# Optimization experiments

Measured on AMD Instinct MI355X. Metric: run time of the kernel, lower is better.

The kernel has to match this reference:

```python
import jax, jax.numpy as jnp
import numpy as np

N_NODES = 50000
N_EDGES = 800000
D_IN = 128
N_HEAD = 4
D_OUT = D_IN // N_HEAD  # 32


def setup_inputs() -> dict:
    key = jax.random.key(0)
    k1, k2, k3, k4, k5 = jax.random.split(key, 5)
    in_feat = jax.random.normal(k1, (N_NODES, D_IN), dtype=jnp.float32)
    edge_ind = jax.random.randint(k2, (2, N_EDGES), 0, N_NODES, dtype=jnp.int64)
    # xavier-ish scaled params
    W_proj = jax.random.normal(k3, (D_IN, N_HEAD * D_OUT), dtype=jnp.float32) * (1.0 / np.sqrt(D_IN))
    a_src = jax.random.normal(k4, (1, N_HEAD, D_OUT), dtype=jnp.float32) * (1.0 / np.sqrt(D_OUT))
    a_tgt = jax.random.normal(k5, (1, N_HEAD, D_OUT), dtype=jnp.float32) * (1.0 / np.sqrt(D_OUT))
    bias = jnp.zeros((N_HEAD * D_OUT,), dtype=jnp.float32)
    return {"in_feat": in_feat, "edge_ind": edge_ind, "edge_len": N_EDGES,
            "W_proj": W_proj, "a_src": a_src, "a_tgt": a_tgt, "bias": bias}


def reference(in_feat, edge_ind, edge_len, W_proj, a_src, a_tgt, bias):
    n_nodes = in_feat.shape[0]
    n_head, d_out = a_src.shape[1], a_src.shape[2]
    # input projection: [N, d_in] @ [d_in, H*D] -> [N, H, D]
    proj_feat = (in_feat @ W_proj).reshape(n_nodes, n_head, d_out)
    # per-node scores [N, H]
    src_score = jnp.sum(proj_feat * a_src, axis=-1)
    tgt_score = jnp.sum(proj_feat * a_tgt, axis=-1)
    src_ind, tgt_ind = edge_ind[0], edge_ind[1]
    # per-edge score [E, H]
    edge_score = jax.nn.leaky_relu(src_score[src_ind] + tgt_score[tgt_ind], negative_slope=0.2)
    edge_score = jnp.exp(edge_score - jnp.max(edge_score))  # global max, as in source
    # segment-softmax denominator via scatter-add over target nodes
    neigh_sums = jax.ops.segment_sum(edge_score, tgt_ind, num_segments=n_nodes)  # [N, H]
    att_per_edge = edge_score / (neigh_sums[tgt_ind] + 1e-16)  # [E, H]
    # weighted aggregation: gather src features, scale, scatter-add to targets
    src_feat_weighted = proj_feat[src_ind] * att_per_edge[..., None]  # [E, H, D]
    out_feat = jax.ops.segment_sum(src_feat_weighted, tgt_ind, num_segments=n_nodes)  # [N, H, D]
    return out_feat.reshape(n_nodes, -1) + bias
```

## Files before the change

### kernel.cpp

```cpp
#include <hip/hip_runtime.h>
#include <hip/hip_bf16.h>

typedef __attribute__((ext_vector_type(8))) short bf16x8;
typedef __attribute__((ext_vector_type(4))) float f32x4;

__device__ __forceinline__ ushort f2bf(float f) {
    unsigned u = __float_as_uint(f);
    return (ushort)((u + 0x7fffu + ((u >> 16) & 1u)) >> 16);
}
__device__ __forceinline__ float blo(unsigned u) { return __uint_as_float(u << 16); }
__device__ __forceinline__ float bhi(unsigned u) { return __uint_as_float(u & 0xffff0000u); }

__global__ void k_wt(const float* __restrict__ W, ushort* __restrict__ Wt) {
    int idx = blockIdx.x * 256 + threadIdx.x;
    int nn = idx >> 7, kk = idx & 127;
    Wt[idx] = f2bf(W[kk * 128 + nn]);
}

__global__ __launch_bounds__(256) void k_proj(const float* __restrict__ A,
                                              const ushort* __restrict__ Wt_g,
                                              const float* __restrict__ a_src,
                                              const float* __restrict__ a_tgt,
                                              ushort* __restrict__ Pb,
                                              float* __restrict__ ss,
                                              float* __restrict__ ts,
                                              int* __restrict__ deg, int n) {
    __shared__ __align__(16) char smem[49152];
    const int tid = threadIdx.x;
    const int row0 = blockIdx.x * 64;

    {
        int gid = blockIdx.x * 256 + tid;
        if (gid < n) deg[gid] = 0;
    }

#pragma unroll
    for (int it = 0; it < 8; ++it) {
        int idx = it * 256 + tid;
        int r   = idx >> 5;
        int kc  = (idx & 31) << 2;
        int gr  = row0 + r;
        float4 v = make_float4(0.f, 0.f, 0.f, 0.f);
        if (gr < n) v = *(const float4*)&A[(size_t)gr * 128 + kc];
        ushort4 pk;
        pk.x = f2bf(v.x); pk.y = f2bf(v.y); pk.z = f2bf(v.z); pk.w = f2bf(v.w);
        *(ushort4*)(smem + ((r * 256 + kc * 2) ^ ((r & 7) << 4))) = pk;
    }
#pragma unroll
    for (int it = 0; it < 8; ++it) {
        int idx = it * 256 + tid;
        int nn  = idx >> 4;
        int k8  = (idx & 15) << 3;
        uint4 v = *(const uint4*)&Wt_g[nn * 128 + k8];
        *(uint4*)(smem + 16384 + ((nn * 256 + k8 * 2) ^ ((nn & 7) << 4))) = v;
    }
    __syncthreads();

    const int l  = tid & 63, w = tid >> 6;
    const int lr = l & 15,  lk = l >> 4;
    const int arow = w * 16 + lr;

    f32x4 acc[8] = {};
#pragma unroll
    for (int ks = 0; ks < 4; ++ks) {
        int kk = ks * 32 + lk * 8;
        bf16x8 af = *(const bf16x8*)(smem + ((arow * 256 + kk * 2) ^ ((arow & 7) << 4)));
#pragma unroll
        for (int nt = 0; nt < 8; ++nt) {
            int nn = nt * 16 + lr;
            bf16x8 bf = *(const bf16x8*)(smem + 16384 + ((nn * 256 + kk * 2) ^ ((nn & 7) << 4)));
            acc[nt] = __builtin_amdgcn_mfma_f32_16x16x32_bf16(af, bf, acc[nt], 0, 0, 0);
        }
    }

#pragma unroll
    for (int nt = 0; nt < 8; ++nt) {
#pragma unroll
        for (int r = 0; r < 4; ++r) {
            int gr = row0 + w * 16 + lk * 4 + r;
            if (gr < n) Pb[(size_t)gr * 128 + nt * 16 + lr] = f2bf(acc[nt][r]);
        }
    }

    float av[8], bw[8];
#pragma unroll
    for (int t = 0; t < 8; ++t) { av[t] = a_src[t * 16 + lr]; bw[t] = a_tgt[t * 16 + lr]; }
#pragma unroll
    for (int r = 0; r < 4; ++r) {
#pragma unroll
        for (int h = 0; h < 4; ++h) {
            float s1 = acc[2 * h][r] * av[2 * h] + acc[2 * h + 1][r] * av[2 * h + 1];
            float s2 = acc[2 * h][r] * bw[2 * h] + acc[2 * h + 1][r] * bw[2 * h + 1];
#pragma unroll
            for (int off = 1; off < 16; off <<= 1) {
                s1 += __shfl_xor(s1, off, 64);
                s2 += __shfl_xor(s2, off, 64);
            }
            if (lr == 0) {
                int gr = row0 + w * 16 + lk * 4 + r;
                if (gr < n) { ss[gr * 4 + h] = s1; ts[gr * 4 + h] = s2; }
            }
        }
    }
}

__global__ void k_hist(const int* __restrict__ tgt, int* __restrict__ deg,
                       int* __restrict__ rank, int E) {
    int e = blockIdx.x * 256 + threadIdx.x;
    if (e < E) rank[e] = atomicAdd(&deg[tgt[e]], 1);
}

__global__ __launch_bounds__(256) void k_scan1(const int* __restrict__ deg,
                                               int* __restrict__ rowptr,
                                               int* __restrict__ sums, int n) {
    __shared__ int sd[256];
    int tid = threadIdx.x;
    int i = blockIdx.x * 256 + tid;
    int v = (i < n) ? deg[i] : 0;
    sd[tid] = v; __syncthreads();
#pragma unroll
    for (int off = 1; off < 256; off <<= 1) {
        int t = (tid >= off) ? sd[tid - off] : 0;
        __syncthreads();
        sd[tid] += t;
        __syncthreads();
    }
    if (i < n) rowptr[i + 1] = sd[tid];
    if (tid == 255) sums[blockIdx.x] = sd[255];
}

__global__ __launch_bounds__(256) void k_scan23(int* __restrict__ rowptr,
                                                const int* __restrict__ sums,
                                                int nchunks, int n) {
    __shared__ int sd[256];
    int tid = threadIdx.x;
    int v = (tid < nchunks) ? sums[tid] : 0;
    sd[tid] = v; __syncthreads();
#pragma unroll
    for (int off = 1; off < 256; off <<= 1) {
        int t = (tid >= off) ? sd[tid - off] : 0;
        __syncthreads();
        sd[tid] += t;
        __syncthreads();
    }
    int b = blockIdx.x;
    int prefix = (b == 0) ? 0 : sd[b - 1];
    int i = b * 256 + tid;
    if (i < n) {
        rowptr[i + 1] += prefix;
        if (i == 0) rowptr[0] = 0;
    }
}

__global__ void k_scatter(const int* __restrict__ src, const int* __restrict__ tgt,
                          const int* __restrict__ rowptr, const int* __restrict__ rank,
                          int* __restrict__ srcs, int E) {
    int e = blockIdx.x * 256 + threadIdx.x;
    if (e >= E) return;
    int t = tgt[e];
    srcs[rowptr[t] + rank[e]] = src[e];
}

__global__ __launch_bounds__(256) void k_aggr(const int* __restrict__ rowptr,
                                              const int* __restrict__ srcs,
                                              const float* __restrict__ ss,
                                              const float* __restrict__ ts,
                                              const ushort* __restrict__ Pb,
                                              const float* __restrict__ bias,
                                              float* __restrict__ out, int n) {
    int node = blockIdx.x * 4 + (threadIdx.x >> 6);
    if (node >= n) return;
    const int lane = threadIdx.x & 63;
    const int c = lane * 2;
    const int h = lane >> 4;
    const float tsc = ts[node * 4 + h];
    int b0 = rowptr[node], b1 = rowptr[node + 1];

    float ax0 = 0.f, ay0 = 0.f, ax1 = 0.f, ay1 = 0.f;
    float ax2 = 0.f, ay2 = 0.f, ax3 = 0.f, ay3 = 0.f;
    float den = 0.f;
    int i = b0;
    for (; i + 3 < b1; i += 4) {
        int s0 = srcs[i], s1 = srcs[i + 1], s2 = srcs[i + 2], s3 = srcs[i + 3];
        float w0 = ss[s0 * 4 + h] + tsc;
        float w1 = ss[s1 * 4 + h] + tsc;
        float w2 = ss[s2 * 4 + h] + tsc;
        float w3 = ss[s3 * 4 + h] + tsc;
        unsigned p0 = *(const unsigned*)&Pb[(size_t)s0 * 128 + c];
        unsigned p1 = *(const unsigned*)&Pb[(size_t)s1 * 128 + c];
        unsigned p2 = *(const unsigned*)&Pb[(size_t)s2 * 128 + c];
        unsigned p3 = *(const unsigned*)&Pb[(size_t)s3 * 128 + c];
        w0 = w0 > 0.f ? w0 : 0.2f * w0;  float e0 = __expf(w0);
        w1 = w1 > 0.f ? w1 : 0.2f * w1;  float e1 = __expf(w1);
        w2 = w2 > 0.f ? w2 : 0.2f * w2;  float e2 = __expf(w2);
        w3 = w3 > 0.f ? w3 : 0.2f * w3;  float e3 = __expf(w3);
        den += (e0 + e1) + (e2 + e3);
        ax0 = fmaf(e0, blo(p0), ax0); ay0 = fmaf(e0, bhi(p0), ay0);
        ax1 = fmaf(e1, blo(p1), ax1); ay1 = fmaf(e1, bhi(p1), ay1);
        ax2 = fmaf(e2, blo(p2), ax2); ay2 = fmaf(e2, bhi(p2), ay2);
        ax3 = fmaf(e3, blo(p3), ax3); ay3 = fmaf(e3, bhi(p3), ay3);
    }
    for (; i < b1; ++i) {
        int s0 = srcs[i];
        float w0 = ss[s0 * 4 + h] + tsc;
        w0 = w0 > 0.f ? w0 : 0.2f * w0;
        float e0 = __expf(w0);
        unsigned p0 = *(const unsigned*)&Pb[(size_t)s0 * 128 + c];
        den += e0;
        ax0 = fmaf(e0, blo(p0), ax0); ay0 = fmaf(e0, bhi(p0), ay0);
    }
    float inv = 1.f / (den + 1e-16f);
    float2 bv = *(const float2*)&bias[c];
    float2 o;
    o.x = ((ax0 + ax1) + (ax2 + ax3)) * inv + bv.x;
    o.y = ((ay0 + ay1) + (ay2 + ay3)) * inv + bv.y;
    *(float2*)&out[(size_t)node * 128 + c] = o;
}

extern "C" void kernel_launch(void* const* d_in, const int* in_sizes, int n_in,
                              void* d_out, int out_size, void* d_ws, size_t ws_size,
                              hipStream_t stream) {
    const float* in_feat = (const float*)d_in[0];
    const int*   edge    = (const int*)d_in[1];
    const float* W_proj  = (const float*)d_in[3];
    const float* a_src   = (const float*)d_in[4];
    const float* a_tgt   = (const float*)d_in[5];
    const float* bias    = (const float*)d_in[6];
    float* out = (float*)d_out;

    const int n = in_sizes[0] / 128;
    const int E = in_sizes[1] / 2;
    const int* src = edge;
    const int* tgt = edge + E;

    ushort* Pb   = (ushort*)d_ws;
    ushort* Wt_g = Pb + (size_t)n * 128;
    float*  ss   = (float*)(Wt_g + 128 * 128);
    float*  ts   = ss + (size_t)n * 4;
    int* deg    = (int*)(ts + (size_t)n * 4);
    int* rowptr = deg + n;
    int* sums   = rowptr + n + 1;
    int* rank   = sums + 256;
    int* srcs   = rank + E;

    const int nchunks = (n + 255) / 256;

    k_wt<<<64, 256, 0, stream>>>(W_proj, Wt_g);
    k_proj<<<(n + 63) / 64, 256, 0, stream>>>(in_feat, Wt_g, a_src, a_tgt,
                                              Pb, ss, ts, deg, n);
    k_hist<<<(E + 255) / 256, 256, 0, stream>>>(tgt, deg, rank, E);
    k_scan1<<<nchunks, 256, 0, stream>>>(deg, rowptr, sums, n);
    k_scan23<<<nchunks, 256, 0, stream>>>(rowptr, sums, nchunks, n);
    k_scatter<<<(E + 255) / 256, 256, 0, stream>>>(src, tgt, rowptr, rank, srcs, E);
    k_aggr<<<(n + 3) / 4, 256, 0, stream>>>(rowptr, srcs, ss, ts, Pb, bias, out, n);
}
```

Before: 127.1 us.

## Fuse histogram into projection, precompute bf16 edge weights, narrow indices to 16-bit

Zeroing of the degree array moves into the weight-transpose kernel, and the histogram becomes extra blocks of the projection launch, removing one kernel. The rank, sorted-source and per-edge exp-score arrays are stored as 16-bit values. The scatter kernel is sharded by destination position and also writes bf16 edge exp scores in CSR order. Aggregation now splits heads across blocks and edge slots across lanes, reading the precomputed scores instead of recomputing them. This cuts gather traffic and exp work in the hot aggregation loop. In exchange, node count and per-node degree must fit in 16 bits, edge weights lose precision, and the scatter reads its inputs eight times.

Result: slower. 201.6 us (+58.6%).

```diff
diff --git a/kernel.cpp b/kernel.cpp
--- a/kernel.cpp
+++ b/kernel.cpp
@@ -8,31 +8,43 @@
     unsigned u = __float_as_uint(f);
     return (ushort)((u + 0x7fffu + ((u >> 16) & 1u)) >> 16);
 }
+__device__ __forceinline__ float bf2f(ushort b) {
+    return __uint_as_float(((unsigned)b) << 16);
+}
 __device__ __forceinline__ float blo(unsigned u) { return __uint_as_float(u << 16); }
 __device__ __forceinline__ float bhi(unsigned u) { return __uint_as_float(u & 0xffff0000u); }
 
-__global__ void k_wt(const float* __restrict__ W, ushort* __restrict__ Wt) {
+__global__ void k_wt(const float* __restrict__ W, ushort* __restrict__ Wt,
+                     int* __restrict__ deg, int n) {
     int idx = blockIdx.x * 256 + threadIdx.x;
-    int nn = idx >> 7, kk = idx & 127;
-    Wt[idx] = f2bf(W[kk * 128 + nn]);
-}
-
-__global__ __launch_bounds__(256) void k_proj(const float* __restrict__ A,
-                                              const ushort* __restrict__ Wt_g,
-                                              const float* __restrict__ a_src,
-                                              const float* __restrict__ a_tgt,
-                                              ushort* __restrict__ Pb,
-                                              float* __restrict__ ss,
-                                              float* __restrict__ ts,
-                                              int* __restrict__ deg, int n) {
+    if (idx < 16384) {
+        int nn = idx >> 7, kk = idx & 127;
+        Wt[idx] = f2bf(W[kk * 128 + nn]);
+    }
+    if (idx < n) deg[idx] = 0;
+}
+
+__global__ __launch_bounds__(256) void k_projhist(const float* __restrict__ A,
+                                                  const ushort* __restrict__ Wt_g,
+                                                  const float* __restrict__ a_src,
+                                                  const float* __restrict__ a_tgt,
+                                                  ushort* __restrict__ Pb,
+                                                  float* __restrict__ ss,
+                                                  float* __restrict__ ts,
+                                                  const int* __restrict__ tgt,
+                                                  int* __restrict__ deg,
+                                                  ushort* __restrict__ rank,
+                                                  int n, int E, int PB) {
     __shared__ __align__(16) char smem[49152];
     const int tid = threadIdx.x;
+
+    if ((int)blockIdx.x >= PB) {
+        int e = ((int)blockIdx.x - PB) * 256 + tid;
+        if (e < E) rank[e] = (ushort)atomicAdd(&deg[tgt[e]], 1);
+        return;
+    }
+
     const int row0 = blockIdx.x * 64;
-
-    {
-        int gid = blockIdx.x * 256 + tid;
-        if (gid < n) deg[gid] = 0;
-    }
 
 #pragma unroll
     for (int it = 0; it < 8; ++it) {
@@ -104,12 +116,6 @@
     }
 }
 
-__global__ void k_hist(const int* __restrict__ tgt, int* __restrict__ deg,
-                       int* __restrict__ rank, int E) {
-    int e = blockIdx.x * 256 + threadIdx.x;
-    if (e < E) rank[e] = atomicAdd(&deg[tgt[e]], 1);
-}
-
 __global__ __launch_bounds__(256) void k_scan1(const int* __restrict__ deg,
                                                int* __restrict__ rowptr,
                                                int* __restrict__ sums, int n) {
@@ -152,69 +158,87 @@
     }
 }
 
-__global__ void k_scatter(const int* __restrict__ src, const int* __restrict__ tgt,
-                          const int* __restrict__ rowptr, const int* __restrict__ rank,
-                          int* __restrict__ srcs, int E) {
-    int e = blockIdx.x * 256 + threadIdx.x;
-    if (e >= E) return;
-    int t = tgt[e];
-    srcs[rowptr[t] + rank[e]] = src[e];
+__global__ __launch_bounds__(256) void k_scatter(const int* __restrict__ src,
+                                                 const int* __restrict__ tgt,
+                                                 const int* __restrict__ rowptr,
+                                                 const ushort* __restrict__ rank,
+                                                 const float* __restrict__ ss,
+                                                 const float* __restrict__ ts,
+                                                 ushort* __restrict__ srcs,
+                                                 ushort* __restrict__ esc, int E) {
+    const int shard = blockIdx.x & 7;
+    const int base  = (blockIdx.x >> 3) * 2048;
+    const int tid = threadIdx.x;
+#pragma unroll
+    for (int j = 0; j < 8; ++j) {
+        int e = base + j * 256 + tid;
+        if (e < E) {
+            int t = tgt[e];
+            int pos = rowptr[t] + rank[e];
+            bool m_src = (((pos >> 5) & 7) == shard);
+            bool m_esc = (((pos >> 3) & 7) == shard);
+            if (m_src | m_esc) {
+                int s = src[e];
+                if (m_src) srcs[pos] = (ushort)s;
+                if (m_esc) {
+                    float4 a = *(const float4*)&ss[s * 4];
+                    float4 b = *(const float4*)&ts[t * 4];
+                    float v; ushort4 r;
+                    v = a.x + b.x; v = v > 0.f ? v : 0.2f * v; r.x = f2bf(__expf(v));
+                    v = a.y + b.y; v = v > 0.f ? v : 0.2f * v; r.y = f2bf(__expf(v));
+                    v = a.z + b.z; v = v > 0.f ? v : 0.2f * v; r.z = f2bf(__expf(v));
+                    v = a.w + b.w; v = v > 0.f ? v : 0.2f * v; r.w = f2bf(__expf(v));
+                    *(ushort4*)&esc[(size_t)pos * 4] = r;
+                }
+            }
+        }
+    }
 }
 
 __global__ __launch_bounds__(256) void k_aggr(const int* __restrict__ rowptr,
-                                              const int* __restrict__ srcs,
-                                              const float* __restrict__ ss,
-                                              const float* __restrict__ ts,
+                                              const int* __restrict__ deg,
+                                              const ushort* __restrict__ srcs,
+                                              const ushort* __restrict__ esc,
                                               const ushort* __restrict__ Pb,
                                               const float* __restrict__ bias,
                                               float* __restrict__ out, int n) {
-    int node = blockIdx.x * 4 + (threadIdx.x >> 6);
+    const int bid = blockIdx.x;
+    const int h = bid & 3;
+    int node = __builtin_amdgcn_readfirstlane(((bid >> 2) << 2) + (threadIdx.x >> 6));
     if (node >= n) return;
     const int lane = threadIdx.x & 63;
-    const int c = lane * 2;
-    const int h = lane >> 4;
-    const float tsc = ts[node * 4 + h];
-    int b0 = rowptr[node], b1 = rowptr[node + 1];
-
-    float ax0 = 0.f, ay0 = 0.f, ax1 = 0.f, ay1 = 0.f;
-    float ax2 = 0.f, ay2 = 0.f, ax3 = 0.f, ay3 = 0.f;
-    float den = 0.f;
-    int i = b0;
-    for (; i + 3 < b1; i += 4) {
-        int s0 = srcs[i], s1 = srcs[i + 1], s2 = srcs[i + 2], s3 = srcs[i + 3];
-        float w0 = ss[s0 * 4 + h] + tsc;
-        float w1 = ss[s1 * 4 + h] + tsc;
-        float w2 = ss[s2 * 4 + h] + tsc;
-        float w3 = ss[s3 * 4 + h] + tsc;
-        unsigned p0 = *(const unsigned*)&Pb[(size_t)s0 * 128 + c];
-        unsigned p1 = *(const unsigned*)&Pb[(size_t)s1 * 128 + c];
-        unsigned p2 = *(const unsigned*)&Pb[(size_t)s2 * 128 + c];
-        unsigned p3 = *(const unsigned*)&Pb[(size_t)s3 * 128 + c];
-        w0 = w0 > 0.f ? w0 : 0.2f * w0;  float e0 = __expf(w0);
-        w1 = w1 > 0.f ? w1 : 0.2f * w1;  float e1 = __expf(w1);
-        w2 = w2 > 0.f ? w2 : 0.2f * w2;  float e2 = __expf(w2);
-        w3 = w3 > 0.f ? w3 : 0.2f * w3;  float e3 = __expf(w3);
-        den += (e0 + e1) + (e2 + e3);
-        ax0 = fmaf(e0, blo(p0), ax0); ay0 = fmaf(e0, bhi(p0), ay0);
-        ax1 = fmaf(e1, blo(p1), ax1); ay1 = fmaf(e1, bhi(p1), ay1);
-        ax2 = fmaf(e2, blo(p2), ax2); ay2 = fmaf(e2, bhi(p2), ay2);
-        ax3 = fmaf(e3, blo(p3), ax3); ay3 = fmaf(e3, bhi(p3), ay3);
-    }
-    for (; i < b1; ++i) {
-        int s0 = srcs[i];
-        float w0 = ss[s0 * 4 + h] + tsc;
-        w0 = w0 > 0.f ? w0 : 0.2f * w0;
-        float e0 = __expf(w0);
-        unsigned p0 = *(const unsigned*)&Pb[(size_t)s0 * 128 + c];
-        den += e0;
-        ax0 = fmaf(e0, blo(p0), ax0); ay0 = fmaf(e0, bhi(p0), ay0);
-    }
-    float inv = 1.f / (den + 1e-16f);
-    float2 bv = *(const float2*)&bias[c];
-    float2 o;
-    o.x = ((ax0 + ax1) + (ax2 + ax3)) * inv + bv.x;
-    o.y = ((ay0 + ay1) + (ay2 + ay3)) * inv + bv.y;
-    *(float2*)&out[(size_t)node * 128 + c] = o;
+    const int slot = lane >> 4;
+    const int q    = lane & 15;
+    const int cidx = h * 32 + q * 2;
+    const int b0 = rowptr[node];
+    const int limit = b0 + deg[node];
+
+    float ax = 0.f, ay = 0.f, den = 0.f;
+    for (int i = b0; i < limit; i += 8) {
+        int ia = i + slot, ib = i + slot + 4;
+        ushort sa = srcs[ia], sb = srcs[ib];
+        bool va = ia < limit, vb = ib < limit;
+        int ma = va ? (int)sa : 0, mb = vb ? (int)sb : 0;
+        unsigned pa = *(const unsigned*)(Pb + (size_t)ma * 128 + cidx);
+        unsigned pb = *(const unsigned*)(Pb + (size_t)mb * 128 + cidx);
+        ushort ua = esc[ia * 4 + h], ub = esc[ib * 4 + h];
+        float ea = va ? bf2f(ua) : 0.f;
+        float eb = vb ? bf2f(ub) : 0.f;
+        den += ea + eb;
+        ax = fmaf(ea, blo(pa), ax); ay = fmaf(ea, bhi(pa), ay);
+        ax = fmaf(eb, blo(pb), ax); ay = fmaf(eb, bhi(pb), ay);
+    }
+    den += __shfl_xor(den, 16, 64); den += __shfl_xor(den, 32, 64);
+    ax  += __shfl_xor(ax, 16, 64);  ax  += __shfl_xor(ax, 32, 64);
+    ay  += __shfl_xor(ay, 16, 64);  ay  += __shfl_xor(ay, 32, 64);
+    if (slot == 0) {
+        float inv = 1.f / (den + 1e-16f);
+        float2 bv = *(const float2*)&bias[cidx];
+        float2 o;
+        o.x = ax * inv + bv.x;
+        o.y = ay * inv + bv.y;
+        *(float2*)&out[(size_t)node * 128 + cidx] = o;
+    }
 }
 
 extern "C" void kernel_launch(void* const* d_in, const int* in_sizes, int n_in,
@@ -233,24 +257,33 @@
     const int* src = edge;
     const int* tgt = edge + E;
 
-    ushort* Pb   = (ushort*)d_ws;
-    ushort* Wt_g = Pb + (size_t)n * 128;
-    float*  ss   = (float*)(Wt_g + 128 * 128);
-    float*  ts   = ss + (size_t)n * 4;
-    int* deg    = (int*)(ts + (size_t)n * 4);
-    int* rowptr = deg + n;
-    int* sums   = rowptr + n + 1;
-    int* rank   = sums + 256;
-    int* srcs   = rank + E;
+    uintptr_t p = (uintptr_t)d_ws;
+    auto alloc = [&](size_t bytes) { uintptr_t r = p; p = (p + bytes + 15) & ~(uintptr_t)15; return r; };
+    float*  ss     = (float*)alloc((size_t)n * 4 * 4);
+    float*  ts     = (float*)alloc((size_t)n * 4 * 4);
+    int*    deg    = (int*)alloc((size_t)n * 4);
+    int*    rowptr = (int*)alloc((size_t)(n + 1) * 4);
+    int*    sums   = (int*)alloc(256 * 4);
+    ushort* Pb     = (ushort*)alloc((size_t)n * 128 * 2);
+    ushort* Wt_g   = (ushort*)alloc(16384 * 2);
+    ushort* rank   = (ushort*)alloc((size_t)E * 2);
+    ushort* srcs   = (ushort*)alloc(((size_t)E + 8) * 2);
+    ushort* esc    = (ushort*)alloc(((size_t)E + 8) * 4 * 2);
 
     const int nchunks = (n + 255) / 256;
-
-    k_wt<<<64, 256, 0, stream>>>(W_proj, Wt_g);
-    k_proj<<<(n + 63) / 64, 256, 0, stream>>>(in_feat, Wt_g, a_src, a_tgt,
-                                              Pb, ss, ts, deg, n);
-    k_hist<<<(E + 255) / 256, 256, 0, stream>>>(tgt, deg, rank, E);
+    const int PB = (n + 63) / 64;
+    const int HB = (E + 255) / 256;
+
+    k_wt<<<(n + 255) / 256, 256, 0, stream>>>(W_proj, Wt_g, deg, n);
+    k_projhist<<<PB + HB, 256, 0, stream>>>(in_feat, Wt_g, a_src, a_tgt,
+                                            Pb, ss, ts, tgt, deg, rank, n, E, PB);
     k_scan1<<<nchunks, 256, 0, stream>>>(deg, rowptr, sums, n);
     k_scan23<<<nchunks, 256, 0, stream>>>(rowptr, sums, nchunks, n);
-    k_scatter<<<(E + 255) / 256, 256, 0, stream>>>(src, tgt, rowptr, rank, srcs, E);
-    k_aggr<<<(n + 3) / 4, 256, 0, stream>>>(rowptr, srcs, ss, ts, Pb, bias, out, n);
-}
+    {
+        int chunks = (E + 2047) / 2048;
+        k_scatter<<<chunks * 8, 256, 0, stream>>>(src, tgt, rowptr, rank,
+                                                  ss, ts, srcs, esc, E);
+    }
+    k_aggr<<<((n + 3) / 4) * 4, 256, 0, stream>>>(rowptr, deg, srcs, esc,
+                                                  Pb, bias, out, n);
+}
```
